# Performance work log

Measured on AMD Instinct MI355X. Metric: run time of the kernel, lower is better.

The kernel has to match this reference:

```python
import jax, jax.numpy as jnp
import numpy as np

NUM_FRAME = 300
LEN_FRAME = 512


def setup_inputs() -> dict:
    key = jax.random.key(0)
    # nervegram: [batch, freq, time, channel]
    nervegram = jax.random.normal(key, (4, 50, 20000, 2), dtype=jnp.float32)
    return {"nervegram": nervegram}


def reference(nervegram):
    # [B, F, T, C] -> [B, F, C, T]
    x = jnp.transpose(nervegram.astype(jnp.float32), (0, 1, 3, 2))
    T = x.shape[-1]

    # frame start indices (static, matches np.linspace(..., dtype=int))
    starts = np.linspace(0, T - LEN_FRAME, NUM_FRAME).astype(np.int64)
    idx = starts[:, None] + np.arange(LEN_FRAME)  # [NUM_FRAME, LEN_FRAME]
    frames = x[..., idx]  # [B, F, C, NUM_FRAME, LEN_FRAME]

    # periodic Hann window (tf.signal.hann_window, periodic=True)
    n = jnp.arange(LEN_FRAME, dtype=jnp.float32)
    window = 0.5 - 0.5 * jnp.cos(2.0 * jnp.pi * n / LEN_FRAME)
    frames = frames * window

    # Wiener-Khinchin autocorrelation: irfft(|rfft(x)|^2)
    spec = jnp.fft.rfft(frames, axis=-1)
    acf = jnp.fft.irfft(spec * jnp.conj(spec), n=LEN_FRAME, axis=-1)
    acf = jax.nn.relu(acf)

    # normalize by sqrt of zero-lag value (guard zeros)
    norm = acf[..., 0:1]
    norm = jnp.where(norm == 0, jnp.ones_like(norm), norm)
    acf = acf / jnp.sqrt(norm)

    # one_sided: keep non-negative lags
    acf = acf[..., : LEN_FRAME // 2]  # [B, F, C, NUM_FRAME, LAGS]

    # channel_mode == 'mean': [B, F, NUM_FRAME, C, LAGS] -> mean over C
    acf = jnp.transpose(acf, (0, 1, 3, 2, 4))
    acf = jnp.mean(acf, axis=-2)  # [B, F, NUM_FRAME, LAGS]
    return acf
```

## Files before the change

### kernel.cpp

```cpp
#include <hip/hip_runtime.h>

#define NUM_FRAME 300
#define LEN_FRAME 512
#define T_LEN     20000

typedef float floatx4 __attribute__((ext_vector_type(4)));
typedef int   intx8   __attribute__((ext_vector_type(8)));
typedef int   int2a   __attribute__((ext_vector_type(2), aligned(4)));
typedef int   int2w   __attribute__((ext_vector_type(2)));
typedef unsigned int uint32;

#define PAIR8  3152

struct alignas(16) WinTab {
    float w[512];
    constexpr WinTab() : w{} {
        for (int n = 0; n < 512; ++n) {
            int mm = (n <= 256) ? n : 512 - n;
            double x = 3.14159265358979323846 * (double)mm / 512.0;
            double t = x, s = x, x2 = x * x;
            for (int i = 1; i <= 10; ++i) { t *= -x2 / (double)((2 * i) * (2 * i + 1)); s += t; }
            w[n] = (float)(32.0 * s * s);
        }
    }
};
__device__ const WinTab wtab{};

__global__ __launch_bounds__(256, 6) void acorr_fp8(const float* __restrict__ in,
                                                    float* __restrict__ out) {
    __shared__ __align__(16) char lds8[8 * PAIR8];

    const int tid = threadIdx.x;
    const int fj  = tid >> 6;
    const int m   = tid & 63;
    const int x0  = 8 * m;

    {
        const int G  = blockIdx.x * 4 + fj;
        const int bc = (int)((unsigned)G / (unsigned)NUM_FRAME);
        const int fr = G - bc * NUM_FRAME;
        const int start = (int)(((unsigned)fr * (unsigned)(T_LEN - LEN_FRAME))
                                / (unsigned)(NUM_FRAME - 1));
        const float2* src = (const float2*)(in + (size_t)2 * ((size_t)bc * T_LEN + start));

        const int cn = (x0 + 8) & 511;

        const float2 v0 = src[x0],     v1 = src[x0 + 1], v2 = src[x0 + 2], v3 = src[x0 + 3];
        const float2 v4 = src[x0 + 4], v5 = src[x0 + 5], v6 = src[x0 + 6], v7 = src[x0 + 7];
        const float2 c0 = src[cn],     c1 = src[cn + 1], c2 = src[cn + 2], c3 = src[cn + 3];

        const floatx4 wva = *(const floatx4*)&wtab.w[x0];
        const floatx4 wvb = *(const floatx4*)&wtab.w[x0 + 4];
        const floatx4 wvc = *(const floatx4*)&wtab.w[cn];

        #pragma unroll
        for (int c = 0; c < 2; ++c) {
            float f0 = (c ? v0.y : v0.x) * wva[0];
            float f1 = (c ? v1.y : v1.x) * wva[1];
            float f2 = (c ? v2.y : v2.x) * wva[2];
            float f3 = (c ? v3.y : v3.x) * wva[3];
            float f4 = (c ? v4.y : v4.x) * wvb[0];
            float f5 = (c ? v5.y : v5.x) * wvb[1];
            float f6 = (c ? v6.y : v6.x) * wvb[2];
            float f7 = (c ? v7.y : v7.x) * wvb[3];
            float g0 = (c ? c0.y : c0.x) * wvc[0];
            float g1 = (c ? c1.y : c1.x) * wvc[1];
            float g2 = (c ? c2.y : c2.x) * wvc[2];
            float g3 = (c ? c3.y : c3.x) * wvc[3];

            int d0 = __builtin_amdgcn_cvt_pk_fp8_f32(f0, f1, 0,  false);
            d0     = __builtin_amdgcn_cvt_pk_fp8_f32(f2, f3, d0, true);
            int d1 = __builtin_amdgcn_cvt_pk_fp8_f32(f4, f5, 0,  false);
            d1     = __builtin_amdgcn_cvt_pk_fp8_f32(f6, f7, d1, true);
            int d2 = __builtin_amdgcn_cvt_pk_fp8_f32(g0, g1, 0,  false);
            d2     = __builtin_amdgcn_cvt_pk_fp8_f32(g2, g3, d2, true);

            char* P = &lds8[(fj * 2 + c) * PAIR8];
            *(int2w*)(P + 240 + x0) = (int2w){d0, d1};
            if (x0 >= 272)
                *(int2w*)(P + x0 - 272) = (int2w){d0, d1};
            if (x0 < 16)
                *(int2w*)(P + 752 + x0) = (int2w){d0, d1};
            *(int2a*)(P + 1012 + x0) = (int2a){d0, d1};
            if (x0 >= 272)
                *(int2a*)(P + 500 + x0) = (int2a){d0, d1};
            #pragma unroll
            for (int s = 1; s < 4; ++s) {
                int e0 = (int)__builtin_amdgcn_alignbyte((uint32)d1, (uint32)d0, (uint32)s);
                int e1 = (int)__builtin_amdgcn_alignbyte((uint32)d2, (uint32)d1, (uint32)s);
                char* Bp = P + 1008 + 536 * s;
                *(int2w*)(Bp + x0) = (int2w){e0, e1};
                if (x0 < 16)
                    *(int2w*)(Bp + x0 + 512) = (int2w){e0, e1};
            }
        }
    }
    __syncthreads();

    const int lane = tid & 63;
    const int il   = lane & 15;
    const int q    = lane >> 4;

    const char* P0 = &lds8[(fj * 2) * PAIR8];
    const char* aP = P0 + (((il & 8) ? 1012 : 240) + 8 * q - 16 * il);
    const int sB = il & 3;
    const char* bP = P0 + ((sB == 0) ? 240 : (1008 + 536 * sB)) + 4 * (il >> 2) + 8 * q;

    floatx4 acc0 = {0.f, 0.f, 0.f, 0.f};
    floatx4 acc1 = {0.f, 0.f, 0.f, 0.f};
    #pragma unroll
    for (int u = 0; u < 4; ++u) {
        const int o = 128 * u;
        {
            int2a a0 = *(const int2a*)(aP + o);
            int2a a1 = *(const int2a*)(aP + o + 32);
            int2a a2 = *(const int2a*)(aP + o + 64);
            int2a a3 = *(const int2a*)(aP + o + 96);
            int2a b0 = *(const int2a*)(bP + o);
            int2a b1 = *(const int2a*)(bP + o + 32);
            int2a b2 = *(const int2a*)(bP + o + 64);
            int2a b3 = *(const int2a*)(bP + o + 96);
            intx8 a = {a0.x, a0.y, a1.x, a1.y, a2.x, a2.y, a3.x, a3.y};
            intx8 b = {b0.x, b0.y, b1.x, b1.y, b2.x, b2.y, b3.x, b3.y};
            acc0 = __builtin_amdgcn_mfma_scale_f32_16x16x128_f8f6f4(
                a, b, acc0, 0, 0, 0, 0x7F7F7F7F, 0, 0x7F7F7F7F);
        }
        {
            int2a a0 = *(const int2a*)(aP + PAIR8 + o);
            int2a a1 = *(const int2a*)(aP + PAIR8 + o + 32);
            int2a a2 = *(const int2a*)(aP + PAIR8 + o + 64);
            int2a a3 = *(const int2a*)(aP + PAIR8 + o + 96);
            int2a b0 = *(const int2a*)(bP + PAIR8 + o);
            int2a b1 = *(const int2a*)(bP + PAIR8 + o + 32);
            int2a b2 = *(const int2a*)(bP + PAIR8 + o + 64);
            int2a b3 = *(const int2a*)(bP + PAIR8 + o + 96);
            intx8 a = {a0.x, a0.y, a1.x, a1.y, a2.x, a2.y, a3.x, a3.y};
            intx8 b = {b0.x, b0.y, b1.x, b1.y, b2.x, b2.y, b3.x, b3.y};
            acc1 = __builtin_amdgcn_mfma_scale_f32_16x16x128_f8f6f4(
                a, b, acc1, 0, 0, 0, 0x7F7F7F7F, 0, 0x7F7F7F7F);
        }
    }

    float n00 = __int_as_float(__builtin_amdgcn_readfirstlane(__float_as_int(acc0[0])));
    float n01 = __int_as_float(__builtin_amdgcn_readfirstlane(__float_as_int(acc1[0])));
    float n0r0 = fmaxf(n00, 0.f);
    float n0r1 = fmaxf(n01, 0.f);
    float inv0 = (n0r0 == 0.f) ? (1.0f / 1024.0f) : (rsqrtf(n0r0) * (1.0f / 32.0f));
    float inv1 = (n0r1 == 0.f) ? (1.0f / 1024.0f) : (rsqrtf(n0r1) * (1.0f / 32.0f));

    const int G = blockIdx.x * 4 + fj;
    float* ob = out + (size_t)G * 256 + q * 64 + il;
    ob[ 0] = 0.5f * (fmaxf(acc0[0], 0.f) * inv0 + fmaxf(acc1[0], 0.f) * inv1);
    ob[16] = 0.5f * (fmaxf(acc0[1], 0.f) * inv0 + fmaxf(acc1[1], 0.f) * inv1);
    ob[32] = 0.5f * (fmaxf(acc0[2], 0.f) * inv0 + fmaxf(acc1[2], 0.f) * inv1);
    ob[48] = 0.5f * (fmaxf(acc0[3], 0.f) * inv0 + fmaxf(acc1[3], 0.f) * inv1);
}

extern "C" void kernel_launch(void* const* d_in, const int* in_sizes, int n_in,
                              void* d_out, int out_size, void* d_ws, size_t ws_size,
                              hipStream_t stream) {
    const float* in = (const float*)d_in[0];
    float* out = (float*)d_out;
    dim3 grid(15000);
    dim3 block(256);
    acorr_fp8<<<grid, block, 0, stream>>>(in, out);
}
```

Measured before the change: 119.2 us.

## Compact fp8 LDS layout and spread wraparound writes across dedicated lanes

Reorganizes the per-channel fp8 LDS staging buffer to a smaller footprint, removing the divergent conditional wraparound stores from each thread. Instead, lanes 0-51 each reload and convert an extra 8-sample segment and write it as one uniform store into the halo or shifted regions. This shrinks shared memory per block, which may allow more resident blocks. In exchange it adds redundant global loads and conversions per thread.

```diff
diff --git a/kernel.cpp b/kernel.cpp
--- a/kernel.cpp
+++ b/kernel.cpp
@@ -10,7 +10,9 @@
 typedef int   int2w   __attribute__((ext_vector_type(2)));
 typedef unsigned int uint32;
 
-#define PAIR8  3152
+#define B1     1288
+#define BSTR   536
+#define PAIR8  2896
 
 struct alignas(16) WinTab {
     float w[512];
@@ -48,10 +50,26 @@
         const float2 v0 = src[x0],     v1 = src[x0 + 1], v2 = src[x0 + 2], v3 = src[x0 + 3];
         const float2 v4 = src[x0 + 4], v5 = src[x0 + 5], v6 = src[x0 + 6], v7 = src[x0 + 7];
         const float2 c0 = src[cn],     c1 = src[cn + 1], c2 = src[cn + 2], c3 = src[cn + 3];
-
         const floatx4 wva = *(const floatx4*)&wtab.w[x0];
         const floatx4 wvb = *(const floatx4*)&wtab.w[x0 + 4];
         const floatx4 wvc = *(const floatx4*)&wtab.w[cn];
+
+        int n0 = 0, laddr = 0, sft = 0;
+        {
+            const int l = m;
+            if (l < 14)      { n0 = 400 + 8 * l;        laddr = 8 * l; }
+            else if (l < 16) { n0 = 8 * (l - 14);       laddr = 624 + 8 * (l - 14); }
+            else if (l < 46) { n0 = 272 + 8 * (l - 16); laddr = 644 + 8 * (l - 16); }
+            else if (l < 52) { const int lh = l - 46, s = 1 + (lh >> 1), h = lh & 1;
+                               n0 = 8 * h; laddr = B1 + BSTR * (s - 1) + 512 + 8 * h; sft = s; }
+        }
+        const int nc2 = sft ? (n0 + 8) : 0;
+        const float2 r0 = src[n0],     r1 = src[n0 + 1], r2 = src[n0 + 2], r3 = src[n0 + 3];
+        const float2 r4 = src[n0 + 4], r5 = src[n0 + 5], r6 = src[n0 + 6], r7 = src[n0 + 7];
+        const float2 s0 = src[nc2],    s1 = src[nc2 + 1], s2 = src[nc2 + 2], s3 = src[nc2 + 3];
+        const floatx4 wra = *(const floatx4*)&wtab.w[n0];
+        const floatx4 wrb = *(const floatx4*)&wtab.w[n0 + 4];
+        const floatx4 wrc = *(const floatx4*)&wtab.w[nc2];
 
         #pragma unroll
         for (int c = 0; c < 2; ++c) {
@@ -67,7 +85,6 @@
             float g1 = (c ? c1.y : c1.x) * wvc[1];
             float g2 = (c ? c2.y : c2.x) * wvc[2];
             float g3 = (c ? c3.y : c3.x) * wvc[3];
-
             int d0 = __builtin_amdgcn_cvt_pk_fp8_f32(f0, f1, 0,  false);
             d0     = __builtin_amdgcn_cvt_pk_fp8_f32(f2, f3, d0, true);
             int d1 = __builtin_amdgcn_cvt_pk_fp8_f32(f4, f5, 0,  false);
@@ -76,22 +93,38 @@
             d2     = __builtin_amdgcn_cvt_pk_fp8_f32(g2, g3, d2, true);
 
             char* P = &lds8[(fj * 2 + c) * PAIR8];
-            *(int2w*)(P + 240 + x0) = (int2w){d0, d1};
-            if (x0 >= 272)
-                *(int2w*)(P + x0 - 272) = (int2w){d0, d1};
-            if (x0 < 16)
-                *(int2w*)(P + 752 + x0) = (int2w){d0, d1};
-            *(int2a*)(P + 1012 + x0) = (int2a){d0, d1};
-            if (x0 >= 272)
-                *(int2a*)(P + 500 + x0) = (int2a){d0, d1};
+            *(int2w*)(P + 112 + x0) = (int2w){d0, d1};
+            if (x0 < 400)
+                *(int2a*)(P + 884 + x0) = (int2a){d0, d1};
             #pragma unroll
             for (int s = 1; s < 4; ++s) {
                 int e0 = (int)__builtin_amdgcn_alignbyte((uint32)d1, (uint32)d0, (uint32)s);
                 int e1 = (int)__builtin_amdgcn_alignbyte((uint32)d2, (uint32)d1, (uint32)s);
-                char* Bp = P + 1008 + 536 * s;
-                *(int2w*)(Bp + x0) = (int2w){e0, e1};
-                if (x0 < 16)
-                    *(int2w*)(Bp + x0 + 512) = (int2w){e0, e1};
+                *(int2w*)(P + B1 + BSTR * (s - 1) + x0) = (int2w){e0, e1};
+            }
+            {
+                float h0 = (c ? r0.y : r0.x) * wra[0];
+                float h1 = (c ? r1.y : r1.x) * wra[1];
+                float h2 = (c ? r2.y : r2.x) * wra[2];
+                float h3 = (c ? r3.y : r3.x) * wra[3];
+                float h4 = (c ? r4.y : r4.x) * wrb[0];
+                float h5 = (c ? r5.y : r5.x) * wrb[1];
+                float h6 = (c ? r6.y : r6.x) * wrb[2];
+                float h7 = (c ? r7.y : r7.x) * wrb[3];
+                float k0 = (c ? s0.y : s0.x) * wrc[0];
+                float k1 = (c ? s1.y : s1.x) * wrc[1];
+                float k2 = (c ? s2.y : s2.x) * wrc[2];
+                float k3 = (c ? s3.y : s3.x) * wrc[3];
+                int q0 = __builtin_amdgcn_cvt_pk_fp8_f32(h0, h1, 0,  false);
+                q0     = __builtin_amdgcn_cvt_pk_fp8_f32(h2, h3, q0, true);
+                int q1 = __builtin_amdgcn_cvt_pk_fp8_f32(h4, h5, 0,  false);
+                q1     = __builtin_amdgcn_cvt_pk_fp8_f32(h6, h7, q1, true);
+                int q2 = __builtin_amdgcn_cvt_pk_fp8_f32(k0, k1, 0,  false);
+                q2     = __builtin_amdgcn_cvt_pk_fp8_f32(k2, k3, q2, true);
+                int e0w = sft ? (int)__builtin_amdgcn_alignbyte((uint32)q1, (uint32)q0, (uint32)sft) : q0;
+                int e1w = sft ? (int)__builtin_amdgcn_alignbyte((uint32)q2, (uint32)q1, (uint32)sft) : q1;
+                if (m < 52)
+                    *(int2a*)(P + laddr) = (int2a){e0w, e1w};
             }
         }
     }
@@ -102,9 +135,9 @@
     const int q    = lane >> 4;
 
     const char* P0 = &lds8[(fj * 2) * PAIR8];
-    const char* aP = P0 + (((il & 8) ? 1012 : 240) + 8 * q - 16 * il);
+    const char* aP = P0 + (((il & 8) ? 884 : 112) + 8 * q - 16 * il);
     const int sB = il & 3;
-    const char* bP = P0 + ((sB == 0) ? 240 : (1008 + 536 * sB)) + 4 * (il >> 2) + 8 * q;
+    const char* bP = P0 + ((sB == 0) ? 112 : (B1 + BSTR * (sB - 1))) + 4 * (il >> 2) + 8 * q;
 
     floatx4 acc0 = {0.f, 0.f, 0.f, 0.f};
     floatx4 acc1 = {0.f, 0.f, 0.f, 0.f};
```

Result: slower. 162.2 us (+36.1%).
